# Optimization experiments

Measured on AMD Instinct MI355X. Metric: run time of the kernel, lower is better.

## Reference

```python
import jax, jax.numpy as jnp
import numpy as np

H = 1024      # hidden_dim
C = 151       # len(obj_classes)
E = 200       # embed_dim (GloVe)
DIN = 2048    # inputs_dim
T = 32        # timesteps
B = 128       # batch size (uniform packed lengths)


def setup_inputs() -> dict:
    key = jax.random.key(0)
    ks = jax.random.split(key, 8)
    sequence_tensor = jax.random.normal(ks[0], (T * B, DIN), dtype=jnp.float32) * 0.1
    labels = jax.random.randint(ks[1], (T * B,), 0, C).astype(jnp.int64)
    embed = jax.random.normal(ks[2], (C + 1, E), dtype=jnp.float32) * 0.1   # obj_embed.weight
    Wi = jax.random.normal(ks[3], (DIN + E, 6 * H), dtype=jnp.float32) * 0.02  # input_linearity
    bi = jnp.zeros((6 * H,), dtype=jnp.float32)
    Ws = jax.random.normal(ks[4], (H, 5 * H), dtype=jnp.float32) * 0.02        # state_linearity
    bs = jnp.zeros((5 * H,), dtype=jnp.float32)
    Wo = jax.random.normal(ks[5], (H, C), dtype=jnp.float32) * 0.02            # out_obj
    bo = jnp.zeros((C,), dtype=jnp.float32)
    return {"sequence_tensor": sequence_tensor, "labels": labels, "embed": embed,
            "Wi": Wi, "bi": bi, "Ws": Ws, "bs": bs, "Wo": Wo, "bo": bo,
            "batch_size": B}


def reference(sequence_tensor, embed, Wi, bi, Ws, bs, Wo, bo, labels, batch_size):
    b = int(batch_size)
    t = sequence_tensor.shape[0] // b
    x = sequence_tensor.reshape(t, b, -1)          # [T, B, DIN] packed timestep-major
    lab = labels.reshape(t, b)                     # [T, B]
    h0 = jnp.zeros((b, H), dtype=sequence_tensor.dtype)
    c0 = jnp.zeros((b, H), dtype=sequence_tensor.dtype)
    e0 = jnp.broadcast_to(embed[0], (b, E))        # 'start' embedding

    def step(carry, inp):
        h, c, pe = carry
        xt, lt = inp
        ti = jnp.concatenate([xt, pe], axis=1)     # [B, DIN+E]
        pi = ti @ Wi + bi                          # [B, 6H]
        ps = h @ Ws + bs                           # [B, 5H]

        def gate(k):
            return pi[:, k * H:(k + 1) * H] + ps[:, k * H:(k + 1) * H]

        i_g = jax.nn.sigmoid(gate(0))
        f_g = jax.nn.sigmoid(gate(1))
        m_i = jnp.tanh(gate(2))
        o_g = jax.nn.sigmoid(gate(3))
        c_new = i_g * m_i + f_g * c
        out = o_g * jnp.tanh(c_new)
        hw = jax.nn.sigmoid(gate(4))
        h_new = hw * out + (1.0 - hw) * pi[:, 5 * H:6 * H]  # highway

        pred = h_new @ Wo + bo                     # [B, C]
        nzp = jnp.argmax(pred[:, 1:], axis=1) + 1  # best non-bg class
        l2e = jnp.where(lt == 0, nzp.astype(lt.dtype), lt)
        pe_new = embed[l2e + 1]                    # feedback embedding
        return (h_new, c_new, pe_new), (pred, l2e)

    _, (dists, comms) = jax.lax.scan(step, (h0, c0, e0), (x, lab))
    return dists.reshape(t * b, C), comms.reshape(t * b)
```

## Files before the change

kernel.cpp:

```cpp
#include <hip/hip_runtime.h>
#include <math.h>

#define H    1024
#define C    151
#define E    200
#define DIN  2048
#define T    32
#define B    128
#define SIXH  (6*H)
#define FIVEH (5*H)
#define KTOT  DIN
#define NEMB  (C+1)

typedef _Float16 f16x8 __attribute__((ext_vector_type(8)));
typedef _Float16 f16x4 __attribute__((ext_vector_type(4)));
typedef float    f32x4 __attribute__((ext_vector_type(4)));

#define GLOAD_LDS16(g, l) __builtin_amdgcn_global_load_lds( \
    (const __attribute__((address_space(1))) unsigned int*)(g), \
    (__attribute__((address_space(3))) unsigned int*)(l), 16, 0, 0)

__global__ void init_kernel(float* h, float* c, _Float16* hhi, _Float16* hlo, int* eidx) {
    int i = blockIdx.x * blockDim.x + threadIdx.x;
    if (i < B * H) {
        h[i] = 0.f; c[i] = 0.f;
        hhi[i] = (_Float16)0.f; hlo[i] = (_Float16)0.f;
    }
    if (i < B) eidx[i] = 0;
}

__global__ void cvt_x(const float* __restrict__ X, _Float16* __restrict__ hi,
                      _Float16* __restrict__ lo) {
    size_t i = ((size_t)blockIdx.x * 256 + threadIdx.x) * 4;
    float4 v = *(const float4*)(X + i);
    f16x4 h, l;
    h.x = (_Float16)v.x; l.x = (_Float16)(v.x - (float)h.x);
    h.y = (_Float16)v.y; l.y = (_Float16)(v.y - (float)h.y);
    h.z = (_Float16)v.z; l.z = (_Float16)(v.z - (float)h.z);
    h.w = (_Float16)v.w; l.w = (_Float16)(v.w - (float)h.w);
    *(f16x4*)(hi + i) = h;
    *(f16x4*)(lo + i) = l;
}

template<int KR, int NC>
__global__ void cvt_wT(const float* __restrict__ W, _Float16* __restrict__ hi,
                       _Float16* __restrict__ lo) {
    __shared__ float tile[32][33];
    int n0 = blockIdx.x * 32, k0 = blockIdx.y * 32;
    int tx = threadIdx.x & 31, ty = threadIdx.x >> 5;
    #pragma unroll
    for (int i = 0; i < 4; ++i) {
        int k = ty + i * 8;
        tile[k][tx] = W[(size_t)(k0 + k) * NC + n0 + tx];
    }
    __syncthreads();
    #pragma unroll
    for (int i = 0; i < 4; ++i) {
        int n = ty + i * 8;
        float v = tile[tx][n];
        _Float16 h = (_Float16)v;
        size_t o = (size_t)(n0 + n) * KR + k0 + tx;
        hi[o] = h;
        lo[o] = (_Float16)(v - (float)h);
    }
}

__global__ void etab_kernel(const float* __restrict__ embed,
                            const float* __restrict__ Wi,
                            float* __restrict__ Etab) {
    int n = blockIdx.x * 256 + threadIdx.x;
    int k = blockIdx.y;
    const float* wp = Wi + (size_t)DIN * SIXH + n;
    const float* ep = embed + k * E;
    float acc = 0.f;
    #pragma unroll 8
    for (int e = 0; e < E; ++e)
        acc = fmaf(ep[e], wp[(size_t)e * SIXH], acc);
    Etab[(size_t)k * SIXH + n] = acc;
}

__global__ __launch_bounds__(256) void big_gemm_mfma(
    const _Float16* __restrict__ Ahi, const _Float16* __restrict__ Alo,
    const _Float16* __restrict__ Bhi, const _Float16* __restrict__ Blo,
    const float* __restrict__ bi, float* __restrict__ P)
{
    __shared__ __align__(16) _Float16 sAh[128 * 32];
    __shared__ __align__(16) _Float16 sAl[128 * 32];
    __shared__ __align__(16) _Float16 sBh[128 * 32];
    __shared__ __align__(16) _Float16 sBl[128 * 32];
    const int tid = threadIdx.x;
    const int n0 = blockIdx.x * 128;
    const int m0 = blockIdx.y * 128;
    const int lane = tid & 63, w = tid >> 6;
    const int wm = (w >> 1) * 64, wn = (w & 1) * 64;
    const int lr = lane & 15, lq = lane >> 4;

    f32x4 acc[4][4];
    #pragma unroll
    for (int i = 0; i < 4; ++i)
        #pragma unroll
        for (int j = 0; j < 4; ++j)
            acc[i][j] = (f32x4){0.f, 0.f, 0.f, 0.f};

    const int row0 = tid >> 2;
    const int kc = tid & 3;

    for (int k0 = 0; k0 < KTOT; k0 += 32) {
        #pragma unroll
        for (int i = 0; i < 2; ++i) {
            int row = row0 + i * 64;
            size_t ga = (size_t)(m0 + row) * KTOT + k0 + kc * 8;
            size_t gb = (size_t)(n0 + row) * KTOT + k0 + kc * 8;
            int loff = (i * 256 + tid) * 8;
            GLOAD_LDS16(Ahi + ga, sAh + loff);
            GLOAD_LDS16(Alo + ga, sAl + loff);
            GLOAD_LDS16(Bhi + gb, sBh + loff);
            GLOAD_LDS16(Blo + gb, sBl + loff);
        }
        __syncthreads();
        f16x8 ah[4], al[4], bh[4], bl[4];
        #pragma unroll
        for (int i = 0; i < 4; ++i) {
            ah[i] = *(const f16x8*)&sAh[(wm + i * 16 + lr) * 32 + lq * 8];
            al[i] = *(const f16x8*)&sAl[(wm + i * 16 + lr) * 32 + lq * 8];
            bh[i] = *(const f16x8*)&sBh[(wn + i * 16 + lr) * 32 + lq * 8];
            bl[i] = *(const f16x8*)&sBl[(wn + i * 16 + lr) * 32 + lq * 8];
        }
        #pragma unroll
        for (int i = 0; i < 4; ++i)
            #pragma unroll
            for (int j = 0; j < 4; ++j) {
                acc[i][j] = __builtin_amdgcn_mfma_f32_16x16x32_f16(ah[i], bh[j], acc[i][j], 0, 0, 0);
                acc[i][j] = __builtin_amdgcn_mfma_f32_16x16x32_f16(ah[i], bl[j], acc[i][j], 0, 0, 0);
                acc[i][j] = __builtin_amdgcn_mfma_f32_16x16x32_f16(al[i], bh[j], acc[i][j], 0, 0, 0);
            }
        __syncthreads();
    }
    #pragma unroll
    for (int i = 0; i < 4; ++i)
        #pragma unroll
        for (int j = 0; j < 4; ++j) {
            int gcol = n0 + wn + j * 16 + lr;
            float bv = bi[gcol];
            #pragma unroll
            for (int r = 0; r < 4; ++r) {
                int grow = m0 + wm + i * 16 + lq * 4 + r;
                P[(size_t)grow * SIXH + gcol] = acc[i][j][r] + bv;
            }
        }
}

__global__ __launch_bounds__(256) void ps_mfma(
    const _Float16* __restrict__ Ahi, const _Float16* __restrict__ Alo,
    const _Float16* __restrict__ Bhi, const _Float16* __restrict__ Blo,
    float* __restrict__ ps)
{
    __shared__ __align__(16) _Float16 sAh[64 * 32];
    __shared__ __align__(16) _Float16 sAl[64 * 32];
    __shared__ __align__(16) _Float16 sBh[64 * 32];
    __shared__ __align__(16) _Float16 sBl[64 * 32];
    const int tid = threadIdx.x;
    const int n0 = blockIdx.x * 64;
    const int m0 = blockIdx.y * 64;
    const int lane = tid & 63, w = tid >> 6;
    const int wm = (w >> 1) * 32, wn = (w & 1) * 32;
    const int lr = lane & 15, lq = lane >> 4;

    f32x4 acc[2][2];
    #pragma unroll
    for (int i = 0; i < 2; ++i)
        #pragma unroll
        for (int j = 0; j < 2; ++j)
            acc[i][j] = (f32x4){0.f, 0.f, 0.f, 0.f};

    const int row = tid >> 2;
    const int kc = tid & 3;

    for (int k0 = 0; k0 < H; k0 += 32) {
        size_t ga = (size_t)(m0 + row) * H + k0 + kc * 8;
        size_t gb = (size_t)(n0 + row) * H + k0 + kc * 8;
        int loff = tid * 8;
        GLOAD_LDS16(Ahi + ga, sAh + loff);
        GLOAD_LDS16(Alo + ga, sAl + loff);
        GLOAD_LDS16(Bhi + gb, sBh + loff);
        GLOAD_LDS16(Blo + gb, sBl + loff);
        __syncthreads();
        f16x8 ah[2], al[2], bh[2], bl[2];
        #pragma unroll
        for (int i = 0; i < 2; ++i) {
            ah[i] = *(const f16x8*)&sAh[(wm + i * 16 + lr) * 32 + lq * 8];
            al[i] = *(const f16x8*)&sAl[(wm + i * 16 + lr) * 32 + lq * 8];
            bh[i] = *(const f16x8*)&sBh[(wn + i * 16 + lr) * 32 + lq * 8];
            bl[i] = *(const f16x8*)&sBl[(wn + i * 16 + lr) * 32 + lq * 8];
        }
        #pragma unroll
        for (int i = 0; i < 2; ++i)
            #pragma unroll
            for (int j = 0; j < 2; ++j) {
                acc[i][j] = __builtin_amdgcn_mfma_f32_16x16x32_f16(ah[i], bh[j], acc[i][j], 0, 0, 0);
                acc[i][j] = __builtin_amdgcn_mfma_f32_16x16x32_f16(ah[i], bl[j], acc[i][j], 0, 0, 0);
                acc[i][j] = __builtin_amdgcn_mfma_f32_16x16x32_f16(al[i], bh[j], acc[i][j], 0, 0, 0);
            }
        __syncthreads();
    }
    #pragma unroll
    for (int i = 0; i < 2; ++i)
        #pragma unroll
        for (int j = 0; j < 2; ++j) {
            int gcol = n0 + wn + j * 16 + lr;
            #pragma unroll
            for (int r = 0; r < 4; ++r) {
                int grow = m0 + wm + i * 16 + lq * 4 + r;
                ps[(size_t)grow * FIVEH + gcol] = acc[i][j][r];
            }
        }
}

__global__ void gate_kernel(const float* __restrict__ P,
                            const float* __restrict__ Etab,
                            const float* __restrict__ ps,
                            const float* __restrict__ bs,
                            const int* __restrict__ eidx,
                            float* __restrict__ h,
                            float* __restrict__ c,
                            _Float16* __restrict__ hhi,
                            _Float16* __restrict__ hlo,
                            int t) {
    int j = blockIdx.x * 256 + threadIdx.x;
    int b = blockIdx.y;
    const float* prow = P + (size_t)(t * B + b) * SIXH;
    const float* erow = Etab + (size_t)eidx[b] * SIXH;
    const float* psr  = ps + (size_t)b * FIVEH;
    float g[5];
    #pragma unroll
    for (int k = 0; k < 5; ++k) {
        int col = k * H + j;
        g[k] = prow[col] + erow[col] + psr[col] + bs[col];
    }
    float pi5 = prow[5 * H + j] + erow[5 * H + j];
    float ig = 1.f / (1.f + expf(-g[0]));
    float fg = 1.f / (1.f + expf(-g[1]));
    float mi = tanhf(g[2]);
    float og = 1.f / (1.f + expf(-g[3]));
    float hw = 1.f / (1.f + expf(-g[4]));
    float cv = c[b * H + j];
    float cn = ig * mi + fg * cv;
    float out = og * tanhf(cn);
    float hn = hw * out + (1.f - hw) * pi5;
    c[b * H + j] = cn;
    h[b * H + j] = hn;
    _Float16 hh = (_Float16)hn;
    hhi[b * H + j] = hh;
    hlo[b * H + j] = (_Float16)(hn - (float)hh);
}

__global__ void pred_kernel(const float* __restrict__ h,
                            const float* __restrict__ Wo,
                            const float* __restrict__ bo,
                            const int* __restrict__ labels,
                            float* __restrict__ dists,
                            float* __restrict__ comms,
                            int* __restrict__ eidx,
                            int t) {
    __shared__ float hs[H];
    __shared__ float vals[256];
    __shared__ int   idxs[256];
    int tid = threadIdx.x;
    int b = blockIdx.x;
    for (int i = tid; i < H / 4; i += 256)
        *(float4*)&hs[i * 4] = *(const float4*)&h[b * H + i * 4];
    __syncthreads();
    float pred = 0.f;
    if (tid < C) {
        pred = bo[tid];
        #pragma unroll 8
        for (int k = 0; k < H; ++k)
            pred = fmaf(hs[k], Wo[k * C + tid], pred);
        dists[(size_t)(t * B + b) * C + tid] = pred;
    }
    vals[tid] = (tid >= 1 && tid < C) ? pred : -1e30f;
    idxs[tid] = tid;
    __syncthreads();
    for (int s = 128; s > 0; s >>= 1) {
        if (tid < s) {
            float v2 = vals[tid + s];
            int   i2 = idxs[tid + s];
            if (v2 > vals[tid] || (v2 == vals[tid] && i2 < idxs[tid])) {
                vals[tid] = v2;
                idxs[tid] = i2;
            }
        }
        __syncthreads();
    }
    if (tid == 0) {
        int nzp = idxs[0];
        int lt = labels[t * B + b];
        int comm = (lt == 0) ? nzp : lt;
        comms[t * B + b] = (float)comm;
        eidx[b] = comm + 1;
    }
}

extern "C" void kernel_launch(void* const* d_in, const int* in_sizes, int n_in,
                              void* d_out, int out_size, void* d_ws, size_t ws_size,
                              hipStream_t stream) {
    const float* X      = (const float*)d_in[0];
    const int*   labels = (const int*)  d_in[1];
    const float* embed  = (const float*)d_in[2];
    const float* Wi     = (const float*)d_in[3];
    const float* bi     = (const float*)d_in[4];
    const float* Ws     = (const float*)d_in[5];
    const float* bs     = (const float*)d_in[6];
    const float* Wo     = (const float*)d_in[7];
    const float* bo     = (const float*)d_in[8];

    char* w = (char*)d_ws;
    float* P      = (float*)w;              w += (size_t)T * B * SIXH * 4;
    float* Etab   = (float*)w;              w += (size_t)NEMB * SIXH * 4;
    float* ps     = (float*)w;              w += (size_t)B * FIVEH * 4;
    float* h      = (float*)w;              w += (size_t)B * H * 4;
    float* c      = (float*)w;              w += (size_t)B * H * 4;
    _Float16* hhi = (_Float16*)w;           w += (size_t)B * H * 2;
    _Float16* hlo = (_Float16*)w;           w += (size_t)B * H * 2;
    int* eidx     = (int*)w;                w += 512;
    _Float16* Xhi = (_Float16*)w;           w += (size_t)T * B * KTOT * 2;
    _Float16* Xlo = (_Float16*)w;           w += (size_t)T * B * KTOT * 2;
    _Float16* WiThi = (_Float16*)w;         w += (size_t)SIXH * KTOT * 2;
    _Float16* WiTlo = (_Float16*)w;         w += (size_t)SIXH * KTOT * 2;
    _Float16* WsThi = (_Float16*)w;         w += (size_t)FIVEH * H * 2;
    _Float16* WsTlo = (_Float16*)w;         w += (size_t)FIVEH * H * 2;

    float* dists = (float*)d_out;
    float* comms = dists + (size_t)T * B * C;

    init_kernel<<<512, 256, 0, stream>>>(h, c, hhi, hlo, eidx);
    cvt_x<<<(T * B * KTOT) / (256 * 4), 256, 0, stream>>>(X, Xhi, Xlo);
    cvt_wT<KTOT, SIXH><<<dim3(SIXH / 32, KTOT / 32), 256, 0, stream>>>(Wi, WiThi, WiTlo);
    cvt_wT<H, FIVEH><<<dim3(FIVEH / 32, H / 32), 256, 0, stream>>>(Ws, WsThi, WsTlo);
    etab_kernel<<<dim3(SIXH / 256, NEMB), 256, 0, stream>>>(embed, Wi, Etab);
    big_gemm_mfma<<<dim3(SIXH / 128, (T * B) / 128), 256, 0, stream>>>(Xhi, Xlo, WiThi, WiTlo, bi, P);

    for (int t = 0; t < T; ++t) {
        ps_mfma<<<dim3(FIVEH / 64, B / 64), 256, 0, stream>>>(hhi, hlo, WsThi, WsTlo, ps);
        gate_kernel<<<dim3(H / 256, B), 256, 0, stream>>>(P, Etab, ps, bs, eidx, h, c, hhi, hlo, t);
        pred_kernel<<<B, 256, 0, stream>>>(h, Wo, bo, labels, dists, comms, eidx, t);
    }
}
```

Baseline: 2.550 ms.

## Fuse recurrent timestep loop into persistent cooperative kernel with LDS-resident Ws

Replaces the 96 per-timestep kernel launches with one persistent cooperative kernel of 160 workgroups that keep their slice of the fp16 hi/lo Ws in LDS and synchronise with grid barriers. The gate and prediction work runs in 128 of the workgroups, keeping the cell state in registers and using a transposed Wo for vectorised dot products. It also adds an XOR swizzle to the LDS layout of the big input GEMM to cut bank conflicts. The cost is two grid-wide syncs per step, with a fallback to the old launch loop if the cooperative launch fails.

```diff
diff --git a/kernel.cpp b/kernel.cpp
--- a/kernel.cpp
+++ b/kernel.cpp
@@ -1,5 +1,8 @@
 #include <hip/hip_runtime.h>
+#include <hip/hip_cooperative_groups.h>
 #include <math.h>
+
+namespace cg = cooperative_groups;
 
 #define H    1024
 #define C    151
@@ -11,6 +14,8 @@
 #define FIVEH (5*H)
 #define KTOT  DIN
 #define NEMB  (C+1)
+#define NWG   160
+#define COLS  32
 
 typedef _Float16 f16x8 __attribute__((ext_vector_type(8)));
 typedef _Float16 f16x4 __attribute__((ext_vector_type(4)));
@@ -63,6 +68,12 @@
         hi[o] = h;
         lo[o] = (_Float16)(v - (float)h);
     }
+}
+
+__global__ void cvt_woT(const float* __restrict__ Wo, float* __restrict__ WoT) {
+    int k = blockIdx.x * 256 + threadIdx.x;
+    for (int c = 0; c < C; ++c)
+        WoT[(size_t)c * H + k] = Wo[(size_t)k * C + c];
 }
 
 __global__ void etab_kernel(const float* __restrict__ embed,
@@ -104,13 +115,15 @@
 
     const int row0 = tid >> 2;
     const int kc = tid & 3;
+    const int kcs = kc ^ ((row0 >> 1) & 3);
+    const int sw = (lq ^ ((lr >> 1) & 3)) * 8;
 
     for (int k0 = 0; k0 < KTOT; k0 += 32) {
         #pragma unroll
         for (int i = 0; i < 2; ++i) {
             int row = row0 + i * 64;
-            size_t ga = (size_t)(m0 + row) * KTOT + k0 + kc * 8;
-            size_t gb = (size_t)(n0 + row) * KTOT + k0 + kc * 8;
+            size_t ga = (size_t)(m0 + row) * KTOT + k0 + kcs * 8;
+            size_t gb = (size_t)(n0 + row) * KTOT + k0 + kcs * 8;
             int loff = (i * 256 + tid) * 8;
             GLOAD_LDS16(Ahi + ga, sAh + loff);
             GLOAD_LDS16(Alo + ga, sAl + loff);
@@ -121,10 +134,10 @@
         f16x8 ah[4], al[4], bh[4], bl[4];
         #pragma unroll
         for (int i = 0; i < 4; ++i) {
-            ah[i] = *(const f16x8*)&sAh[(wm + i * 16 + lr) * 32 + lq * 8];
-            al[i] = *(const f16x8*)&sAl[(wm + i * 16 + lr) * 32 + lq * 8];
-            bh[i] = *(const f16x8*)&sBh[(wn + i * 16 + lr) * 32 + lq * 8];
-            bl[i] = *(const f16x8*)&sBl[(wn + i * 16 + lr) * 32 + lq * 8];
+            ah[i] = *(const f16x8*)&sAh[(wm + i * 16 + lr) * 32 + sw];
+            al[i] = *(const f16x8*)&sAl[(wm + i * 16 + lr) * 32 + sw];
+            bh[i] = *(const f16x8*)&sBh[(wn + i * 16 + lr) * 32 + sw];
+            bl[i] = *(const f16x8*)&sBl[(wn + i * 16 + lr) * 32 + sw];
         }
         #pragma unroll
         for (int i = 0; i < 4; ++i)
@@ -148,6 +161,172 @@
                 P[(size_t)grow * SIXH + gcol] = acc[i][j][r] + bv;
             }
         }
+}
+
+__global__ __launch_bounds__(256) void fused_loop(
+    const float* __restrict__ P,
+    const float* __restrict__ Etab,
+    const float* __restrict__ bs,
+    const _Float16* __restrict__ WsThi,
+    const _Float16* __restrict__ WsTlo,
+    _Float16* __restrict__ hhi,
+    _Float16* __restrict__ hlo,
+    float* __restrict__ ps,
+    const float* __restrict__ WoT,
+    const float* __restrict__ bo,
+    const int* __restrict__ labels,
+    float* __restrict__ dists,
+    float* __restrict__ comms)
+{
+    __shared__ __align__(16) _Float16 sBh[COLS * H];
+    __shared__ __align__(16) _Float16 sBl[COLS * H];
+    __shared__ __align__(16) float hs[H];
+    __shared__ float vals[256];
+    __shared__ int   idxs[256];
+    __shared__ int   s_eidx;
+
+    cg::grid_group grid = cg::this_grid();
+    const int wg  = blockIdx.x;
+    const int tid = threadIdx.x;
+    const int n0  = wg * COLS;
+    const int lane = tid & 63, w = tid >> 6;
+    const int lr = lane & 15, lq = lane >> 4;
+
+    for (int gi = tid; gi < COLS * (H / 8); gi += 256) {
+        int col = gi >> 7;
+        int kg  = gi & 127;
+        int dst = (col * (H * 2) + kg * 16) ^ ((col & 7) << 4);
+        *(f16x8*)((char*)sBh + dst) = *(const f16x8*)&WsThi[(size_t)(n0 + col) * H + kg * 8];
+        *(f16x8*)((char*)sBl + dst) = *(const f16x8*)&WsTlo[(size_t)(n0 + col) * H + kg * 8];
+    }
+
+    float creg[4] = {0.f, 0.f, 0.f, 0.f};
+    float bsr[4][5];
+    if (wg < B) {
+        #pragma unroll
+        for (int jj = 0; jj < 4; ++jj)
+            #pragma unroll
+            for (int k = 0; k < 5; ++k)
+                bsr[jj][k] = bs[k * H + jj * 256 + tid];
+    }
+    if (tid == 0) s_eidx = 0;
+    grid.sync();
+
+    const int mrow0 = w * 32;
+
+    for (int t = 0; t < T; ++t) {
+        f32x4 acc[2][2];
+        #pragma unroll
+        for (int i = 0; i < 2; ++i)
+            #pragma unroll
+            for (int j = 0; j < 2; ++j)
+                acc[i][j] = (f32x4){0.f, 0.f, 0.f, 0.f};
+
+        #pragma unroll 2
+        for (int k0 = 0; k0 < H; k0 += 32) {
+            f16x8 ah[2], al[2], bh[2], bl[2];
+            #pragma unroll
+            for (int i = 0; i < 2; ++i) {
+                size_t ho = (size_t)(mrow0 + i * 16 + lr) * H + k0 + lq * 8;
+                ah[i] = *(const f16x8*)&hhi[ho];
+                al[i] = *(const f16x8*)&hlo[ho];
+            }
+            #pragma unroll
+            for (int j = 0; j < 2; ++j) {
+                int col = j * 16 + lr;
+                int off = (col * (H * 2) + (k0 + lq * 8) * 2) ^ ((col & 7) << 4);
+                bh[j] = *(const f16x8*)((const char*)sBh + off);
+                bl[j] = *(const f16x8*)((const char*)sBl + off);
+            }
+            #pragma unroll
+            for (int i = 0; i < 2; ++i)
+                #pragma unroll
+                for (int j = 0; j < 2; ++j) {
+                    acc[i][j] = __builtin_amdgcn_mfma_f32_16x16x32_f16(ah[i], bh[j], acc[i][j], 0, 0, 0);
+                    acc[i][j] = __builtin_amdgcn_mfma_f32_16x16x32_f16(ah[i], bl[j], acc[i][j], 0, 0, 0);
+                    acc[i][j] = __builtin_amdgcn_mfma_f32_16x16x32_f16(al[i], bh[j], acc[i][j], 0, 0, 0);
+                }
+        }
+        #pragma unroll
+        for (int i = 0; i < 2; ++i)
+            #pragma unroll
+            for (int j = 0; j < 2; ++j)
+                #pragma unroll
+                for (int r = 0; r < 4; ++r)
+                    ps[(size_t)(mrow0 + i * 16 + lq * 4 + r) * FIVEH + n0 + j * 16 + lr] = acc[i][j][r];
+
+        grid.sync();
+
+        if (wg < B) {
+            const int b = wg;
+            const float* prow = P + (size_t)(t * B + b) * SIXH;
+            const float* erow = Etab + (size_t)s_eidx * SIXH;
+            const float* psr  = ps + (size_t)b * FIVEH;
+            #pragma unroll
+            for (int jj = 0; jj < 4; ++jj) {
+                int j = jj * 256 + tid;
+                float gv[5];
+                #pragma unroll
+                for (int k = 0; k < 5; ++k) {
+                    int col = k * H + j;
+                    gv[k] = prow[col] + erow[col] + psr[col] + bsr[jj][k];
+                }
+                float pi5 = prow[5 * H + j] + erow[5 * H + j];
+                float ig = 1.f / (1.f + expf(-gv[0]));
+                float fg = 1.f / (1.f + expf(-gv[1]));
+                float mi = tanhf(gv[2]);
+                float og = 1.f / (1.f + expf(-gv[3]));
+                float hw = 1.f / (1.f + expf(-gv[4]));
+                float cn = ig * mi + fg * creg[jj];
+                float out = og * tanhf(cn);
+                float hn = hw * out + (1.f - hw) * pi5;
+                creg[jj] = cn;
+                hs[j] = hn;
+                _Float16 hh = (_Float16)hn;
+                hhi[(size_t)b * H + j] = hh;
+                hlo[(size_t)b * H + j] = (_Float16)(hn - (float)hh);
+            }
+            __syncthreads();
+            float predv = 0.f;
+            if (tid < C) {
+                const float* wp = WoT + (size_t)tid * H;
+                float a0 = bo[tid], a1 = 0.f, a2 = 0.f, a3 = 0.f;
+                #pragma unroll 4
+                for (int k = 0; k < H; k += 4) {
+                    float4 w4 = *(const float4*)&wp[k];
+                    float4 h4 = *(const float4*)&hs[k];
+                    a0 = fmaf(h4.x, w4.x, a0);
+                    a1 = fmaf(h4.y, w4.y, a1);
+                    a2 = fmaf(h4.z, w4.z, a2);
+                    a3 = fmaf(h4.w, w4.w, a3);
+                }
+                predv = (a0 + a1) + (a2 + a3);
+                dists[(size_t)(t * B + b) * C + tid] = predv;
+            }
+            vals[tid] = (tid >= 1 && tid < C) ? predv : -1e30f;
+            idxs[tid] = tid;
+            __syncthreads();
+            for (int s = 128; s > 0; s >>= 1) {
+                if (tid < s) {
+                    float v2 = vals[tid + s];
+                    int   i2 = idxs[tid + s];
+                    if (v2 > vals[tid] || (v2 == vals[tid] && i2 < idxs[tid])) {
+                        vals[tid] = v2;
+                        idxs[tid] = i2;
+                    }
+                }
+                __syncthreads();
+            }
+            if (tid == 0) {
+                int nzp = idxs[0];
+                int lt = labels[t * B + b];
+                int comm = (lt == 0) ? nzp : lt;
+                comms[t * B + b] = (float)comm;
+                s_eidx = comm + 1;
+            }
+        }
+        grid.sync();
+    }
 }
 
 __global__ __launch_bounds__(256) void ps_mfma(
@@ -262,20 +441,20 @@
                             float* __restrict__ comms,
                             int* __restrict__ eidx,
                             int t) {
-    __shared__ float hs[H];
+    __shared__ float hsb[H];
     __shared__ float vals[256];
     __shared__ int   idxs[256];
     int tid = threadIdx.x;
     int b = blockIdx.x;
     for (int i = tid; i < H / 4; i += 256)
-        *(float4*)&hs[i * 4] = *(const float4*)&h[b * H + i * 4];
+        *(float4*)&hsb[i * 4] = *(const float4*)&h[b * H + i * 4];
     __syncthreads();
     float pred = 0.f;
     if (tid < C) {
         pred = bo[tid];
         #pragma unroll 8
         for (int k = 0; k < H; ++k)
-            pred = fmaf(hs[k], Wo[k * C + tid], pred);
+            pred = fmaf(hsb[k], Wo[k * C + tid], pred);
         dists[(size_t)(t * B + b) * C + tid] = pred;
     }
     vals[tid] = (tid >= 1 && tid < C) ? pred : -1e30f;
@@ -329,6 +508,7 @@
     _Float16* WiTlo = (_Float16*)w;         w += (size_t)SIXH * KTOT * 2;
     _Float16* WsThi = (_Float16*)w;         w += (size_t)FIVEH * H * 2;
     _Float16* WsTlo = (_Float16*)w;         w += (size_t)FIVEH * H * 2;
+    float* WoT    = (float*)Xhi;
 
     float* dists = (float*)d_out;
     float* comms = dists + (size_t)T * B * C;
@@ -339,10 +519,18 @@
     cvt_wT<H, FIVEH><<<dim3(FIVEH / 32, H / 32), 256, 0, stream>>>(Ws, WsThi, WsTlo);
     etab_kernel<<<dim3(SIXH / 256, NEMB), 256, 0, stream>>>(embed, Wi, Etab);
     big_gemm_mfma<<<dim3(SIXH / 128, (T * B) / 128), 256, 0, stream>>>(Xhi, Xlo, WiThi, WiTlo, bi, P);
-
-    for (int t = 0; t < T; ++t) {
-        ps_mfma<<<dim3(FIVEH / 64, B / 64), 256, 0, stream>>>(hhi, hlo, WsThi, WsTlo, ps);
-        gate_kernel<<<dim3(H / 256, B), 256, 0, stream>>>(P, Etab, ps, bs, eidx, h, c, hhi, hlo, t);
-        pred_kernel<<<B, 256, 0, stream>>>(h, Wo, bo, labels, dists, comms, eidx, t);
-    }
-}
+    cvt_woT<<<dim3(H / 256), 256, 0, stream>>>(Wo, WoT);
+
+    void* args[] = {(void*)&P, (void*)&Etab, (void*)&bs, (void*)&WsThi, (void*)&WsTlo,
+                    (void*)&hhi, (void*)&hlo, (void*)&ps, (void*)&WoT, (void*)&bo,
+                    (void*)&labels, (void*)&dists, (void*)&comms};
+    hipError_t err = hipLaunchCooperativeKernel((void*)fused_loop, dim3(NWG), dim3(256),
+                                                args, 0, stream);
+    if (err != hipSuccess) {
+        for (int t = 0; t < T; ++t) {
+            ps_mfma<<<dim3(FIVEH / 64, B / 64), 256, 0, stream>>>(hhi, hlo, WsThi, WsTlo, ps);
+            gate_kernel<<<dim3(H / 256, B), 256, 0, stream>>>(P, Etab, ps, bs, eidx, h, c, hhi, hlo, t);
+            pred_kernel<<<B, 256, 0, stream>>>(h, Wo, bo, labels, dists, comms, eidx, t);
+        }
+    }
+}
```

After: 3.091 ms. +21.2%, slower.
